# Optimization experiments

Hardware: AMD Instinct MI355X
Metric: run time of the kernel (lower is better)

The kernel has to match this reference:

```python
import jax, jax.numpy as jnp
import numpy as np

NUM_EXPERTS = 8
NUM_SHARED = 1
TOP_K = 2
H = 1024
FF = 4096


def mlp(x, w_gate, w_up, w_down):
    # SmolLM2/LLaMA-style SwiGLU MLP: down( silu(gate(x)) * up(x) )
    g = jax.nn.silu(x @ w_gate)
    u = x @ w_up
    return (g * u) @ w_down


def setup_inputs() -> dict:
    key = jax.random.key(0)
    ks = jax.random.split(key, 2 + 3 * NUM_EXPERTS)
    x = jax.random.normal(ks[0], (4, 2048, H), dtype=jnp.float32)
    w_router = jax.random.normal(ks[1], (H, NUM_EXPERTS), dtype=jnp.float32) * (1.0 / np.sqrt(H))
    # stacked expert weights: [E, H, FF], [E, H, FF], [E, FF, H]
    w_gate = jax.random.normal(ks[2], (NUM_EXPERTS, H, FF), dtype=jnp.float32) * (1.0 / np.sqrt(H))
    w_up = jax.random.normal(ks[3], (NUM_EXPERTS, H, FF), dtype=jnp.float32) * (1.0 / np.sqrt(H))
    w_down = jax.random.normal(ks[4], (NUM_EXPERTS, FF, H), dtype=jnp.float32) * (1.0 / np.sqrt(FF))
    return {"x": x, "w_router": w_router, "w_gate": w_gate, "w_up": w_up, "w_down": w_down}


def reference(x, w_router, w_gate, w_up, w_down):
    B, T, C = x.shape
    router_logits = x @ w_router  # [B,T,E]
    router_probs = jax.nn.softmax(router_logits, axis=-1)
    scores, expert_indices = jax.lax.top_k(router_probs, TOP_K)  # [B,T,K]
    scores = scores / jnp.sum(scores, axis=-1, keepdims=True)

    # Build dense combine weights [B,T,E]: sum of normalized scores where expert selected
    one_hot = jax.nn.one_hot(expert_indices, NUM_EXPERTS, dtype=x.dtype)  # [B,T,K,E]
    combine = jnp.einsum('btk,btke->bte', scores, one_hot)  # [B,T,E]

    # Run every expert on all tokens that selected it; faithful math via dense
    # per-expert compute weighted by combine coefficients.
    def per_expert(e):
        out_e = mlp(x, w_gate[e], w_up[e], w_down[e])  # [B,T,C]
        return out_e * combine[..., e:e+1]

    final_output = jnp.zeros_like(x)
    for e in range(NUM_EXPERTS):
        final_output = final_output + per_expert(e)

    # Losses: original accumulates the same quantity num_experts times in the loop
    z_loss_single = jnp.mean(jnp.square(router_logits))
    probs_mean = jnp.mean(router_probs, axis=(0, 1))  # [E]
    aux_single = NUM_EXPERTS * jnp.mean(probs_mean * jnp.log(probs_mean + 1e-9))
    router_z_loss = jnp.array([NUM_EXPERTS * z_loss_single])
    router_aux_loss = jnp.array([NUM_EXPERTS * aux_single])
    return final_output, router_z_loss, router_aux_loss
```

## Files before the change

### kernel.cpp

```cpp
#include <hip/hip_runtime.h>
#include <stdint.h>

#define NT 8192
#define HD 1024
#define FF 4096
#define NE 8
#define TOTROWS (NT * 2)

typedef __attribute__((ext_vector_type(4))) float v4f;
typedef __attribute__((ext_vector_type(8))) short v8s;

__device__ __forceinline__ unsigned short f2bf(float f) {
    union { float f; uint32_t u; } v; v.f = f;
    uint32_t r = v.u + 0x7FFFu + ((v.u >> 16) & 1u);
    return (unsigned short)(r >> 16);
}
__device__ __forceinline__ float bf2f(unsigned short h) {
    union { uint32_t u; float f; } v; v.u = ((uint32_t)h) << 16;
    return v.f;
}
__device__ __forceinline__ uint32_t pk2(unsigned short a, unsigned short b) {
    return (uint32_t)a | ((uint32_t)b << 16);
}

#define WS_CNT   0ull
#define WS_PZ    1024ull
#define WS_PP    (WS_PZ + 8192ull)
#define WS_PLAN  (WS_PP + 65536ull)
#define WS_IDX   (WS_PLAN + 1024ull)
#define WS_SLOT1 (WS_IDX + 262144ull)
#define WS_W1    (WS_SLOT1 + 32768ull)
#define WS_SLOT2 (WS_W1 + 32768ull)
#define WS_W2    (WS_SLOT2 + 32768ull)
#define WS_XB    (WS_W2 + 32768ull)
#define WS_HBUF  (WS_XB + 16777216ull)
#define WS_DBUF  (WS_HBUF + 134217728ull)
#define WS_WGB   (WS_DBUF + 33554432ull)
#define WS_WUB   (WS_WGB + 67108864ull)
#define WS_WDB   (WS_WUB + 67108864ull)
#define WS_PC_END (WS_WDB + 67108864ull)

__global__ __launch_bounds__(256) void router_kernel(
    const float* __restrict__ x, const float* __restrict__ wr,
    int* __restrict__ cnt, float* __restrict__ pz, float* __restrict__ pp,
    int* __restrict__ idx_list,
    int* __restrict__ slot1, float* __restrict__ w1a,
    int* __restrict__ slot2, float* __restrict__ w2a,
    unsigned short* __restrict__ xb)
{
    __shared__ float sp[4][8];
    __shared__ float sz[4];
    __shared__ int   si[4][2];
    __shared__ float sw[4][2];

    int wave = threadIdx.x >> 6, lane = threadIdx.x & 63;
    int t = blockIdx.x * 4 + wave;
    const float* xr = x + (size_t)t * HD;
    float l[NE];
#pragma unroll
    for (int e = 0; e < NE; e++) l[e] = 0.f;
#pragma unroll
    for (int c = 0; c < 4; c++) {
        int idx4 = c * 64 + lane;
        v4f xv = ((const v4f*)xr)[idx4];
        int h0 = idx4 * 4;
        ushort4 bb;
        bb.x = f2bf(xv[0]); bb.y = f2bf(xv[1]); bb.z = f2bf(xv[2]); bb.w = f2bf(xv[3]);
        ((ushort4*)(xb + (size_t)t * HD))[idx4] = bb;
#pragma unroll
        for (int j = 0; j < 4; j++) {
            const float* wrow = wr + (size_t)(h0 + j) * NE;
            v4f wa = ((const v4f*)wrow)[0];
            v4f wb = ((const v4f*)wrow)[1];
            float xx = xv[j];
            l[0] += xx * wa[0]; l[1] += xx * wa[1]; l[2] += xx * wa[2]; l[3] += xx * wa[3];
            l[4] += xx * wb[0]; l[5] += xx * wb[1]; l[6] += xx * wb[2]; l[7] += xx * wb[3];
        }
    }
#pragma unroll
    for (int e = 0; e < NE; e++) {
#pragma unroll
        for (int off = 32; off >= 1; off >>= 1) l[e] += __shfl_xor(l[e], off);
    }
    if (lane == 0) {
        float mx = l[0];
#pragma unroll
        for (int e = 1; e < NE; e++) mx = fmaxf(mx, l[e]);
        float p[NE]; float s = 0.f;
#pragma unroll
        for (int e = 0; e < NE; e++) { p[e] = __expf(l[e] - mx); s += p[e]; }
        float inv = 1.f / s;
        float zz = 0.f;
#pragma unroll
        for (int e = 0; e < NE; e++) { p[e] *= inv; zz += l[e] * l[e]; sp[wave][e] = p[e]; }
        sz[wave] = zz;
        int i1 = 0;
#pragma unroll
        for (int e = 1; e < NE; e++) if (p[e] > p[i1]) i1 = e;
        int i2 = (i1 == 0) ? 1 : 0;
#pragma unroll
        for (int e = 0; e < NE; e++) if (e != i1 && p[e] > p[i2]) i2 = e;
        float d = p[i1] + p[i2];
        si[wave][0] = i1; sw[wave][0] = p[i1] / d;
        si[wave][1] = i2; sw[wave][1] = p[i2] / d;
    }
    __syncthreads();
    int tid = threadIdx.x;
    if (tid < 8)
        pp[blockIdx.x * 8 + tid] = sp[0][tid] + sp[1][tid] + sp[2][tid] + sp[3][tid];
    else if (tid == 8)
        pz[blockIdx.x] = sz[0] + sz[1] + sz[2] + sz[3];
    if (tid == 0) {
        int cl[8] = {0,0,0,0,0,0,0,0};
        int bl[8];
#pragma unroll
        for (int w = 0; w < 4; w++) { cl[si[w][0]]++; cl[si[w][1]]++; }
#pragma unroll
        for (int ee = 0; ee < 8; ee++)
            if (cl[ee]) { bl[ee] = atomicAdd(&cnt[ee * 32], cl[ee]); cl[ee] = 0; }
#pragma unroll
        for (int w = 0; w < 4; w++) {
            int tok = blockIdx.x * 4 + w;
#pragma unroll
            for (int k = 0; k < 2; k++) {
                int ee = si[w][k];
                int pos = bl[ee] + cl[ee]++;
                idx_list[ee * NT + pos] = tok;
                if (k == 0) { slot1[tok] = (ee << 16) | pos; w1a[tok] = sw[w][0]; }
                else        { slot2[tok] = (ee << 16) | pos; w2a[tok] = sw[w][1]; }
            }
        }
    }
}

__global__ __launch_bounds__(256) void loss_plan_kernel(
    const float* __restrict__ pz, const float* __restrict__ pp,
    const int* __restrict__ cnt, int* __restrict__ plan, float* __restrict__ out)
{
    int tid = threadIdx.x;
    if (tid == 0) {
        int nm = 0, off = 0;
        for (int e = 0; e < NE; e++) {
            plan[4 + e] = off;
            int c = cnt[e * 32];
            int nb = (c + 127) >> 7;
            for (int mb = 0; mb < nb; mb++) plan[16 + nm++] = (e << 16) | mb;
            off += c;
        }
        plan[4 + NE] = off;
        plan[0] = nm;
    }
    float z = 0.f, p[8] = {0.f,0.f,0.f,0.f,0.f,0.f,0.f,0.f};
    for (int b = tid; b < 2048; b += 256) {
        z += pz[b];
#pragma unroll
        for (int e = 0; e < 8; e++) p[e] += pp[b * 8 + e];
    }
#pragma unroll
    for (int off = 32; off >= 1; off >>= 1) {
        z += __shfl_xor(z, off);
#pragma unroll
        for (int e = 0; e < 8; e++) p[e] += __shfl_xor(p[e], off);
    }
    __shared__ float red[4][9];
    int wave = tid >> 6, lane = tid & 63;
    if (lane == 0) {
        red[wave][0] = z;
#pragma unroll
        for (int e = 0; e < 8; e++) red[wave][1 + e] = p[e];
    }
    __syncthreads();
    if (tid == 0) {
        float zz = red[0][0] + red[1][0] + red[2][0] + red[3][0];
        float s = 0.f;
        for (int e = 0; e < 8; e++) {
            float pm = (red[0][1+e] + red[1][1+e] + red[2][1+e] + red[3][1+e]) / (float)NT;
            s += pm * logf(pm + 1e-9f);
        }
        out[(size_t)NT * HD]     = 8.f * zz / (float)(NT * NE);
        out[(size_t)NT * HD + 1] = 8.f * s;
    }
}

template<int K, int N>
__global__ __launch_bounds__(256) void conv_kernel(
    const float* __restrict__ src, unsigned short* __restrict__ dst)
{
    __shared__ float t[64][65];
    int tid = threadIdx.x;
    int e = blockIdx.z;
    int r = tid >> 2, q = tid & 3;
    const float* s = src + ((size_t)e * K + blockIdx.y * 64 + r) * N + blockIdx.x * 64 + q * 16;
#pragma unroll
    for (int j = 0; j < 4; j++) {
        v4f v = *(const v4f*)(s + j * 4);
        t[r][q * 16 + j * 4 + 0] = v[0];
        t[r][q * 16 + j * 4 + 1] = v[1];
        t[r][q * 16 + j * 4 + 2] = v[2];
        t[r][q * 16 + j * 4 + 3] = v[3];
    }
    __syncthreads();
    unsigned short b[16];
#pragma unroll
    for (int i = 0; i < 16; i++) b[i] = f2bf(t[q * 16 + i][r]);
    uint4 o0, o1;
    o0.x = pk2(b[0], b[1]);  o0.y = pk2(b[2], b[3]);
    o0.z = pk2(b[4], b[5]);  o0.w = pk2(b[6], b[7]);
    o1.x = pk2(b[8], b[9]);  o1.y = pk2(b[10], b[11]);
    o1.z = pk2(b[12], b[13]); o1.w = pk2(b[14], b[15]);
    unsigned short* d = dst + ((size_t)e * N + blockIdx.x * 64 + r) * K + blockIdx.y * 64 + q * 16;
    *(uint4*)d = o0;
    *(uint4*)(d + 8) = o1;
}

template<bool PC>
__global__ __launch_bounds__(256) void gateup_kernel(
    const void* __restrict__ Bg_, const void* __restrict__ Bu_,
    const int* __restrict__ plan, const int* __restrict__ idx_list,
    const unsigned short* __restrict__ xb, unsigned short* __restrict__ Hbuf)
{
    constexpr int LDA = 72;
    __shared__ unsigned short Asm[128 * LDA];
    __shared__ unsigned short Bsm[2][64 * LDA];
    __shared__ int toks[128];

    if ((int)blockIdx.y >= plan[0]) return;
    int tbv = plan[16 + blockIdx.y];
    int e = tbv >> 16, mb = tbv & 0xffff;
    int hbase = plan[4 + e];
    int n_e = plan[5 + e] - hbase;
    int m0 = mb * 128;
    int n0 = blockIdx.x * 64;
    int tid = threadIdx.x, lane = tid & 63, wave = tid >> 6;
    int wm = wave >> 1, wn = wave & 1;

    if (tid < 128) {
        int r = m0 + tid;
        toks[tid] = idx_list[e * NT + ((r < n_e) ? r : 0)];
    }
    __syncthreads();

    v4f acc[2][4][2];
#pragma unroll
    for (int w = 0; w < 2; w++)
#pragma unroll
        for (int i = 0; i < 4; i++)
#pragma unroll
            for (int j = 0; j < 2; j++) acc[w][i][j] = (v4f){0.f, 0.f, 0.f, 0.f};

    int am = tid >> 1, ah = tid & 1;
    const unsigned short* Arow = xb + (size_t)toks[am] * HD;
    int brow = tid >> 3, bch = tid & 7;

    for (int k0 = 0; k0 < HD; k0 += 64) {
        {
            const uint4* src = (const uint4*)(Arow + k0 + ah * 32);
            uint4* dst = (uint4*)(Asm + am * LDA + ah * 32);
#pragma unroll
            for (int j = 0; j < 4; j++) dst[j] = src[j];
        }
        if constexpr (PC) {
#pragma unroll
            for (int w = 0; w < 2; w++) {
                const unsigned short* wsl = (const unsigned short*)(w ? Bu_ : Bg_);
#pragma unroll
                for (int p = 0; p < 2; p++) {
                    int row = p * 32 + brow;
                    *(uint4*)(Bsm[w] + row * LDA + bch * 8) =
                        *(const uint4*)(wsl + ((size_t)e * FF + n0 + row) * HD + k0 + bch * 8);
                }
            }
        } else {
            int n = (tid & 15) * 4, kg = tid >> 4;
#pragma unroll
            for (int w = 0; w < 2; w++) {
                const float* bp = (const float*)(w ? Bu_ : Bg_)
                    + (size_t)e * HD * FF + (size_t)(k0 + kg * 4) * FF + n0 + n;
                v4f rr[4];
#pragma unroll
                for (int kk = 0; kk < 4; kk++) rr[kk] = *(const v4f*)(bp + (size_t)kk * FF);
#pragma unroll
                for (int c = 0; c < 4; c++) {
                    uint2 p2;
                    p2.x = pk2(f2bf(rr[0][c]), f2bf(rr[1][c]));
                    p2.y = pk2(f2bf(rr[2][c]), f2bf(rr[3][c]));
                    *(uint2*)(Bsm[w] + (n + c) * LDA + kg * 4) = p2;
                }
            }
        }
        __syncthreads();
        {
            int q = lane >> 4, ln = lane & 15;
#pragma unroll
            for (int ks = 0; ks < 2; ks++) {
                v8s a[4], b[2][2];
#pragma unroll
                for (int i = 0; i < 4; i++)
                    a[i] = *(const v8s*)(Asm + (wm * 64 + i * 16 + ln) * LDA + ks * 32 + q * 8);
#pragma unroll
                for (int w = 0; w < 2; w++)
#pragma unroll
                    for (int j = 0; j < 2; j++)
                        b[w][j] = *(const v8s*)(Bsm[w] + (wn * 32 + j * 16 + ln) * LDA + ks * 32 + q * 8);
#pragma unroll
                for (int i = 0; i < 4; i++)
#pragma unroll
                    for (int j = 0; j < 2; j++) {
                        acc[0][i][j] = __builtin_amdgcn_mfma_f32_16x16x32_bf16(a[i], b[0][j], acc[0][i][j], 0, 0, 0);
                        acc[1][i][j] = __builtin_amdgcn_mfma_f32_16x16x32_bf16(a[i], b[1][j], acc[1][i][j], 0, 0, 0);
                    }
            }
        }
        __syncthreads();
    }

    int q = lane >> 4, ln = lane & 15;
#pragma unroll
    for (int i = 0; i < 4; i++)
#pragma unroll
        for (int j = 0; j < 2; j++)
#pragma unroll
            for (int r = 0; r < 4; r++) {
                int lm = wm * 64 + i * 16 + q * 4 + r;
                int gm = m0 + lm;
                int gn = n0 + wn * 32 + j * 16 + ln;
                if (gm < n_e) {
                    float g = acc[0][i][j][r];
                    float u = acc[1][i][j][r];
                    float sg = g / (1.f + __expf(-g));
                    Hbuf[(size_t)(hbase + gm) * FF + gn] = f2bf(sg * u);
                }
            }
}

template<bool PC>
__global__ __launch_bounds__(256) void down_kernel(
    const void* __restrict__ Bd_, const int* __restrict__ plan,
    const unsigned short* __restrict__ Hbuf, unsigned short* __restrict__ Dbuf)
{
    constexpr int LDA = 72;
    __shared__ unsigned short Asm[128 * LDA];
    __shared__ unsigned short Bsm[128 * LDA];

    if ((int)blockIdx.y >= plan[0]) return;
    int tbv = plan[16 + blockIdx.y];
    int e = tbv >> 16, mb = tbv & 0xffff;
    int hbase = plan[4 + e];
    int n_e = plan[5 + e] - hbase;
    int m0 = mb * 128;
    int n0 = blockIdx.x * 128;
    int tid = threadIdx.x, lane = tid & 63, wave = tid >> 6;
    int wm = wave >> 1, wn = wave & 1;

    v4f acc[4][4];
#pragma unroll
    for (int i = 0; i < 4; i++)
#pragma unroll
        for (int j = 0; j < 4; j++) acc[i][j] = (v4f){0.f, 0.f, 0.f, 0.f};

    int am = tid >> 1, ah = tid & 1;
    const unsigned short* Arow = Hbuf + (size_t)(hbase + m0 + am) * FF;
    int brow = tid >> 3, bch = tid & 7;

    for (int k0 = 0; k0 < FF; k0 += 64) {
        {
            const uint4* src = (const uint4*)(Arow + k0 + ah * 32);
            uint4* dst = (uint4*)(Asm + am * LDA + ah * 32);
#pragma unroll
            for (int j = 0; j < 4; j++) dst[j] = src[j];
        }
        if constexpr (PC) {
            const unsigned short* wsl = (const unsigned short*)Bd_;
#pragma unroll
            for (int p = 0; p < 4; p++) {
                int row = p * 32 + brow;
                *(uint4*)(Bsm + row * LDA + bch * 8) =
                    *(const uint4*)(wsl + ((size_t)e * HD + n0 + row) * FF + k0 + bch * 8);
            }
        } else {
            int n = (tid & 31) * 4, kg = tid >> 5;
            const float* bp = (const float*)Bd_
                + (size_t)e * FF * HD + (size_t)(k0 + kg * 8) * HD + n0 + n;
            v4f rr[8];
#pragma unroll
            for (int kk = 0; kk < 8; kk++) rr[kk] = *(const v4f*)(bp + (size_t)kk * HD);
#pragma unroll
            for (int c = 0; c < 4; c++) {
                uint4 pkd;
                pkd.x = pk2(f2bf(rr[0][c]), f2bf(rr[1][c]));
                pkd.y = pk2(f2bf(rr[2][c]), f2bf(rr[3][c]));
                pkd.z = pk2(f2bf(rr[4][c]), f2bf(rr[5][c]));
                pkd.w = pk2(f2bf(rr[6][c]), f2bf(rr[7][c]));
                *(uint4*)(Bsm + (n + c) * LDA + kg * 8) = pkd;
            }
        }
        __syncthreads();
        {
            int q = lane >> 4, ln = lane & 15;
#pragma unroll
            for (int ks = 0; ks < 2; ks++) {
                v8s a[4], b[4];
#pragma unroll
                for (int i = 0; i < 4; i++)
                    a[i] = *(const v8s*)(Asm + (wm * 64 + i * 16 + ln) * LDA + ks * 32 + q * 8);
#pragma unroll
                for (int j = 0; j < 4; j++)
                    b[j] = *(const v8s*)(Bsm + (wn * 64 + j * 16 + ln) * LDA + ks * 32 + q * 8);
#pragma unroll
                for (int i = 0; i < 4; i++)
#pragma unroll
                    for (int j = 0; j < 4; j++)
                        acc[i][j] = __builtin_amdgcn_mfma_f32_16x16x32_bf16(a[i], b[j], acc[i][j], 0, 0, 0);
            }
        }
        __syncthreads();
    }

    int q = lane >> 4, ln = lane & 15;
#pragma unroll
    for (int i = 0; i < 4; i++)
#pragma unroll
        for (int j = 0; j < 4; j++)
#pragma unroll
            for (int r = 0; r < 4; r++) {
                int lm = wm * 64 + i * 16 + q * 4 + r;
                int gm = m0 + lm;
                int gn = n0 + wn * 64 + j * 16 + ln;
                if (gm < n_e)
                    Dbuf[(size_t)(hbase + gm) * HD + gn] = f2bf(acc[i][j][r]);
            }
}

__global__ __launch_bounds__(256) void gather_kernel(
    const int* __restrict__ slot1, const float* __restrict__ w1a,
    const int* __restrict__ slot2, const float* __restrict__ w2a,
    const int* __restrict__ plan, const unsigned short* __restrict__ Dbuf,
    float* __restrict__ out)
{
    int t = blockIdx.x, c = threadIdx.x;
    int s1 = slot1[t], s2 = slot2[t];
    int h1 = plan[4 + (s1 >> 16)] + (s1 & 0xffff);
    int h2 = plan[4 + (s2 >> 16)] + (s2 & 0xffff);
    float a = w1a[t], b = w2a[t];
    ushort4 d1 = ((const ushort4*)(Dbuf + (size_t)h1 * HD))[c];
    ushort4 d2 = ((const ushort4*)(Dbuf + (size_t)h2 * HD))[c];
    v4f o;
    o[0] = a * bf2f(d1.x) + b * bf2f(d2.x);
    o[1] = a * bf2f(d1.y) + b * bf2f(d2.y);
    o[2] = a * bf2f(d1.z) + b * bf2f(d2.z);
    o[3] = a * bf2f(d1.w) + b * bf2f(d2.w);
    ((v4f*)(out + (size_t)t * HD))[c] = o;
}

extern "C" void kernel_launch(void* const* d_in, const int* in_sizes, int n_in,
                              void* d_out, int out_size, void* d_ws, size_t ws_size,
                              hipStream_t stream)
{
    const float* x  = (const float*)d_in[0];
    const float* wr = (const float*)d_in[1];
    const float* wg = (const float*)d_in[2];
    const float* wu = (const float*)d_in[3];
    const float* wd = (const float*)d_in[4];
    float* out = (float*)d_out;

    char* ws = (char*)d_ws;
    int*   cnt      = (int*)(ws + WS_CNT);
    float* pz       = (float*)(ws + WS_PZ);
    float* pp       = (float*)(ws + WS_PP);
    int*   plan     = (int*)(ws + WS_PLAN);
    int*   idx_list = (int*)(ws + WS_IDX);
    int*   slot1    = (int*)(ws + WS_SLOT1);
    float* w1a      = (float*)(ws + WS_W1);
    int*   slot2    = (int*)(ws + WS_SLOT2);
    float* w2a      = (float*)(ws + WS_W2);
    unsigned short* xb   = (unsigned short*)(ws + WS_XB);
    unsigned short* Hbuf = (unsigned short*)(ws + WS_HBUF);
    unsigned short* Dbuf = (unsigned short*)(ws + WS_DBUF);
    unsigned short* wgb  = (unsigned short*)(ws + WS_WGB);
    unsigned short* wub  = (unsigned short*)(ws + WS_WUB);
    unsigned short* wdb  = (unsigned short*)(ws + WS_WDB);

    bool pc = ws_size >= WS_PC_END;

    hipMemsetAsync(ws + WS_CNT, 0, 1024, stream);

    if (pc) {
        conv_kernel<HD, FF><<<dim3(FF / 64, HD / 64, NE), 256, 0, stream>>>(wg, wgb);
        conv_kernel<HD, FF><<<dim3(FF / 64, HD / 64, NE), 256, 0, stream>>>(wu, wub);
        conv_kernel<FF, HD><<<dim3(HD / 64, FF / 64, NE), 256, 0, stream>>>(wd, wdb);
    }

    router_kernel<<<NT / 4, 256, 0, stream>>>(x, wr, cnt, pz, pp, idx_list,
                                              slot1, w1a, slot2, w2a, xb);
    loss_plan_kernel<<<1, 256, 0, stream>>>(pz, pp, cnt, plan, out);

    if (pc) {
        gateup_kernel<true><<<dim3(FF / 64, 136), 256, 0, stream>>>(
            wgb, wub, plan, idx_list, xb, Hbuf);
        down_kernel<true><<<dim3(HD / 128, 136), 256, 0, stream>>>(
            wdb, plan, Hbuf, Dbuf);
    } else {
        gateup_kernel<false><<<dim3(FF / 64, 136), 256, 0, stream>>>(
            wg, wu, plan, idx_list, xb, Hbuf);
        down_kernel<false><<<dim3(HD / 128, 136), 256, 0, stream>>>(
            wd, plan, Hbuf, Dbuf);
    }

    gather_kernel<<<NT, 256, 0, stream>>>(slot1, w1a, slot2, w2a, plan, Dbuf, out);
}
```

Measured before the change: 1.030 ms.

## Load GEMM tiles directly to LDS with XOR-swizzled unpadded layout

Replaces the register-staged global-to-LDS copies in the gate/up and down expert GEMMs with direct global_load_lds 16-byte transfers. The padded LDS rows (stride 72) become unpadded 64-element rows using an XOR swizzle on 16-byte chunks to avoid bank conflicts, and the fp32 fallback path writes with the same swizzle. The aim is to cut VGPR traffic and instruction count in the load phase and shrink LDS usage. It relies on correct vmcnt handling before the barrier and on the swizzle mapping matching between writers and MFMA fragment readers.

```diff
diff --git a/kernel.cpp b/kernel.cpp
--- a/kernel.cpp
+++ b/kernel.cpp
@@ -21,6 +21,12 @@
 }
 __device__ __forceinline__ uint32_t pk2(unsigned short a, unsigned short b) {
     return (uint32_t)a | ((uint32_t)b << 16);
+}
+__device__ __forceinline__ void gld16(const void* g, void* l) {
+    __builtin_amdgcn_global_load_lds(
+        (const __attribute__((address_space(1))) unsigned int*)g,
+        (__attribute__((address_space(3))) unsigned int*)l,
+        16, 0, 0);
 }
 
 #define WS_CNT   0ull
@@ -213,15 +219,15 @@
     *(uint4*)(d + 8) = o1;
 }
 
+
 template<bool PC>
 __global__ __launch_bounds__(256) void gateup_kernel(
     const void* __restrict__ Bg_, const void* __restrict__ Bu_,
     const int* __restrict__ plan, const int* __restrict__ idx_list,
     const unsigned short* __restrict__ xb, unsigned short* __restrict__ Hbuf)
 {
-    constexpr int LDA = 72;
-    __shared__ unsigned short Asm[128 * LDA];
-    __shared__ unsigned short Bsm[2][64 * LDA];
+    __shared__ unsigned short Asm[128 * 64];
+    __shared__ unsigned short Bsm[2][64 * 64];
     __shared__ int toks[128];
 
     if ((int)blockIdx.y >= plan[0]) return;
@@ -248,28 +254,37 @@
 #pragma unroll
             for (int j = 0; j < 2; j++) acc[w][i][j] = (v4f){0.f, 0.f, 0.f, 0.f};
 
-    int am = tid >> 1, ah = tid & 1;
-    const unsigned short* Arow = xb + (size_t)toks[am] * HD;
-    int brow = tid >> 3, bch = tid & 7;
+    int l8 = lane >> 3, c8 = lane & 7;
+    int srcc = c8 ^ l8;
+    const char* aga[4];
+    unsigned short* ald[4];
+#pragma unroll
+    for (int t = 0; t < 4; t++) {
+        int lr = wave * 32 + t * 8 + l8;
+        aga[t] = (const char*)(xb + (size_t)toks[lr] * HD) + srcc * 16;
+        ald[t] = Asm + (wave * 32 + t * 8) * 64;
+    }
+    int wsel = wave & 1, rb = (wave >> 1) * 32;
+    const unsigned short* wslab = (const unsigned short*)(wsel ? Bu_ : Bg_);
+    const char* bga[4];
+    unsigned short* bld[4];
+    if constexpr (PC) {
+#pragma unroll
+        for (int t = 0; t < 4; t++) {
+            int lr = rb + t * 8 + l8;
+            bga[t] = (const char*)(wslab + ((size_t)e * FF + n0 + lr) * HD) + srcc * 16;
+            bld[t] = Bsm[wsel] + (rb + t * 8) * 64;
+        }
+    }
+
+    int q = lane >> 4, ln = lane & 15, sw8 = ln & 7;
 
     for (int k0 = 0; k0 < HD; k0 += 64) {
-        {
-            const uint4* src = (const uint4*)(Arow + k0 + ah * 32);
-            uint4* dst = (uint4*)(Asm + am * LDA + ah * 32);
-#pragma unroll
-            for (int j = 0; j < 4; j++) dst[j] = src[j];
-        }
+#pragma unroll
+        for (int t = 0; t < 4; t++) gld16(aga[t] + (size_t)k0 * 2, ald[t]);
         if constexpr (PC) {
 #pragma unroll
-            for (int w = 0; w < 2; w++) {
-                const unsigned short* wsl = (const unsigned short*)(w ? Bu_ : Bg_);
-#pragma unroll
-                for (int p = 0; p < 2; p++) {
-                    int row = p * 32 + brow;
-                    *(uint4*)(Bsm[w] + row * LDA + bch * 8) =
-                        *(const uint4*)(wsl + ((size_t)e * FF + n0 + row) * HD + k0 + bch * 8);
-                }
-            }
+            for (int t = 0; t < 4; t++) gld16(bga[t] + (size_t)k0 * 2, bld[t]);
         } else {
             int n = (tid & 15) * 4, kg = tid >> 4;
 #pragma unroll
@@ -284,37 +299,35 @@
                     uint2 p2;
                     p2.x = pk2(f2bf(rr[0][c]), f2bf(rr[1][c]));
                     p2.y = pk2(f2bf(rr[2][c]), f2bf(rr[3][c]));
-                    *(uint2*)(Bsm[w] + (n + c) * LDA + kg * 4) = p2;
+                    char* dstp = (char*)Bsm[w] + (n + c) * 128
+                               + (((kg >> 1) ^ ((n + c) & 7)) * 16) + (kg & 1) * 8;
+                    *(uint2*)dstp = p2;
                 }
             }
         }
         __syncthreads();
-        {
-            int q = lane >> 4, ln = lane & 15;
-#pragma unroll
-            for (int ks = 0; ks < 2; ks++) {
-                v8s a[4], b[2][2];
-#pragma unroll
-                for (int i = 0; i < 4; i++)
-                    a[i] = *(const v8s*)(Asm + (wm * 64 + i * 16 + ln) * LDA + ks * 32 + q * 8);
-#pragma unroll
-                for (int w = 0; w < 2; w++)
-#pragma unroll
-                    for (int j = 0; j < 2; j++)
-                        b[w][j] = *(const v8s*)(Bsm[w] + (wn * 32 + j * 16 + ln) * LDA + ks * 32 + q * 8);
-#pragma unroll
-                for (int i = 0; i < 4; i++)
-#pragma unroll
-                    for (int j = 0; j < 2; j++) {
-                        acc[0][i][j] = __builtin_amdgcn_mfma_f32_16x16x32_bf16(a[i], b[0][j], acc[0][i][j], 0, 0, 0);
-                        acc[1][i][j] = __builtin_amdgcn_mfma_f32_16x16x32_bf16(a[i], b[1][j], acc[1][i][j], 0, 0, 0);
-                    }
-            }
+#pragma unroll
+        for (int ks = 0; ks < 2; ks++) {
+            v8s a[4], b[2][2];
+#pragma unroll
+            for (int i = 0; i < 4; i++)
+                a[i] = *(const v8s*)(Asm + (wm * 64 + i * 16 + ln) * 64 + ((ks * 4 + q) ^ sw8) * 8);
+#pragma unroll
+            for (int w = 0; w < 2; w++)
+#pragma unroll
+                for (int j = 0; j < 2; j++)
+                    b[w][j] = *(const v8s*)(Bsm[w] + (wn * 32 + j * 16 + ln) * 64 + ((ks * 4 + q) ^ sw8) * 8);
+#pragma unroll
+            for (int i = 0; i < 4; i++)
+#pragma unroll
+                for (int j = 0; j < 2; j++) {
+                    acc[0][i][j] = __builtin_amdgcn_mfma_f32_16x16x32_bf16(a[i], b[0][j], acc[0][i][j], 0, 0, 0);
+                    acc[1][i][j] = __builtin_amdgcn_mfma_f32_16x16x32_bf16(a[i], b[1][j], acc[1][i][j], 0, 0, 0);
+                }
         }
         __syncthreads();
     }
 
-    int q = lane >> 4, ln = lane & 15;
 #pragma unroll
     for (int i = 0; i < 4; i++)
 #pragma unroll
@@ -338,9 +351,8 @@
     const void* __restrict__ Bd_, const int* __restrict__ plan,
     const unsigned short* __restrict__ Hbuf, unsigned short* __restrict__ Dbuf)
 {
-    constexpr int LDA = 72;
-    __shared__ unsigned short Asm[128 * LDA];
-    __shared__ unsigned short Bsm[128 * LDA];
+    __shared__ unsigned short Asm[128 * 64];
+    __shared__ unsigned short Bsm[128 * 64];
 
     if ((int)blockIdx.y >= plan[0]) return;
     int tbv = plan[16 + blockIdx.y];
@@ -358,25 +370,36 @@
 #pragma unroll
         for (int j = 0; j < 4; j++) acc[i][j] = (v4f){0.f, 0.f, 0.f, 0.f};
 
-    int am = tid >> 1, ah = tid & 1;
-    const unsigned short* Arow = Hbuf + (size_t)(hbase + m0 + am) * FF;
-    int brow = tid >> 3, bch = tid & 7;
+    int l8 = lane >> 3, c8 = lane & 7;
+    int srcc = c8 ^ l8;
+    const char* aga[4];
+    unsigned short* ald[4];
+    const char* bga[4];
+    unsigned short* bld[4];
+#pragma unroll
+    for (int t = 0; t < 4; t++) {
+        int lr = wave * 32 + t * 8 + l8;
+        aga[t] = (const char*)(Hbuf + (size_t)(hbase + m0 + lr) * FF) + srcc * 16;
+        ald[t] = Asm + (wave * 32 + t * 8) * 64;
+    }
+    if constexpr (PC) {
+#pragma unroll
+        for (int t = 0; t < 4; t++) {
+            int lr = wave * 32 + t * 8 + l8;
+            bga[t] = (const char*)((const unsigned short*)Bd_
+                   + ((size_t)e * HD + n0 + lr) * FF) + srcc * 16;
+            bld[t] = Bsm + (wave * 32 + t * 8) * 64;
+        }
+    }
+
+    int q = lane >> 4, ln = lane & 15, sw8 = ln & 15 & 7;
 
     for (int k0 = 0; k0 < FF; k0 += 64) {
-        {
-            const uint4* src = (const uint4*)(Arow + k0 + ah * 32);
-            uint4* dst = (uint4*)(Asm + am * LDA + ah * 32);
-#pragma unroll
-            for (int j = 0; j < 4; j++) dst[j] = src[j];
-        }
+#pragma unroll
+        for (int t = 0; t < 4; t++) gld16(aga[t] + (size_t)k0 * 2, ald[t]);
         if constexpr (PC) {
-            const unsigned short* wsl = (const unsigned short*)Bd_;
-#pragma unroll
-            for (int p = 0; p < 4; p++) {
-                int row = p * 32 + brow;
-                *(uint4*)(Bsm + row * LDA + bch * 8) =
-                    *(const uint4*)(wsl + ((size_t)e * HD + n0 + row) * FF + k0 + bch * 8);
-            }
+#pragma unroll
+            for (int t = 0; t < 4; t++) gld16(bga[t] + (size_t)k0 * 2, bld[t]);
         } else {
             int n = (tid & 31) * 4, kg = tid >> 5;
             const float* bp = (const float*)Bd_
@@ -391,32 +414,29 @@
                 pkd.y = pk2(f2bf(rr[2][c]), f2bf(rr[3][c]));
                 pkd.z = pk2(f2bf(rr[4][c]), f2bf(rr[5][c]));
                 pkd.w = pk2(f2bf(rr[6][c]), f2bf(rr[7][c]));
-                *(uint4*)(Bsm + (n + c) * LDA + kg * 8) = pkd;
+                char* dstp = (char*)Bsm + (n + c) * 128 + ((kg ^ ((n + c) & 7)) * 16);
+                *(uint4*)dstp = pkd;
             }
         }
         __syncthreads();
-        {
-            int q = lane >> 4, ln = lane & 15;
-#pragma unroll
-            for (int ks = 0; ks < 2; ks++) {
-                v8s a[4], b[4];
-#pragma unroll
-                for (int i = 0; i < 4; i++)
-                    a[i] = *(const v8s*)(Asm + (wm * 64 + i * 16 + ln) * LDA + ks * 32 + q * 8);
+#pragma unroll
+        for (int ks = 0; ks < 2; ks++) {
+            v8s a[4], b[4];
+#pragma unroll
+            for (int i = 0; i < 4; i++)
+                a[i] = *(const v8s*)(Asm + (wm * 64 + i * 16 + ln) * 64 + ((ks * 4 + q) ^ sw8) * 8);
+#pragma unroll
+            for (int j = 0; j < 4; j++)
+                b[j] = *(const v8s*)(Bsm + (wn * 64 + j * 16 + ln) * 64 + ((ks * 4 + q) ^ sw8) * 8);
+#pragma unroll
+            for (int i = 0; i < 4; i++)
 #pragma unroll
                 for (int j = 0; j < 4; j++)
-                    b[j] = *(const v8s*)(Bsm + (wn * 64 + j * 16 + ln) * LDA + ks * 32 + q * 8);
-#pragma unroll
-                for (int i = 0; i < 4; i++)
-#pragma unroll
-                    for (int j = 0; j < 4; j++)
-                        acc[i][j] = __builtin_amdgcn_mfma_f32_16x16x32_bf16(a[i], b[j], acc[i][j], 0, 0, 0);
-            }
+                    acc[i][j] = __builtin_amdgcn_mfma_f32_16x16x32_bf16(a[i], b[j], acc[i][j], 0, 0, 0);
         }
         __syncthreads();
     }
 
-    int q = lane >> 4, ln = lane & 15;
 #pragma unroll
     for (int i = 0; i < 4; i++)
 #pragma unroll
```

New measurement: 1.081 ms. +5.0%, slower.
